# Kernel optimization log

Hardware: AMD Instinct MI355X
Metric: run time of the kernel (lower is better)

## Reference

```python
import jax, jax.numpy as jnp
import numpy as np

N_NODES = 100000
N_EDGES = 1600000
F_IN, F_HID, F_OUT = 128, 128, 16


def _add_self_loops(edge_index, n):
    loop = jnp.arange(n, dtype=edge_index.dtype)
    src = jnp.concatenate([edge_index[0], loop])
    dst = jnp.concatenate([edge_index[1], loop])
    return src, dst


def _gcn_conv(x, W, b, src, dst, n):
    # linear transform first (PyG/jraphx GCNConv order)
    h = x @ W  # [N, out]
    # symmetric normalization with unit edge weights, degrees on dst (incl. self loops)
    ones = jnp.ones(src.shape[0], dtype=h.dtype)
    deg = jax.ops.segment_sum(ones, dst, num_segments=n)
    dinv = jnp.where(deg > 0, jax.lax.rsqrt(deg), jnp.zeros((), h.dtype))
    norm = dinv[src] * dinv[dst]  # [E']
    msg = h[src] * norm[:, None]  # gather + scale: [E', out]
    out = jax.ops.segment_sum(msg, dst, num_segments=n)  # scatter-add
    return out + b


def setup_inputs() -> dict:
    key = jax.random.key(0)
    k1, k2, k3, k4, k5, k6 = jax.random.split(key, 6)
    x = jax.random.normal(k1, (N_NODES, F_IN), dtype=jnp.float32)
    edge_index = jax.random.randint(k2, (2, N_EDGES), 0, N_NODES, dtype=jnp.int32)
    W1 = jax.random.normal(k3, (F_IN, F_HID), dtype=jnp.float32) * (1.0 / np.sqrt(F_IN))
    b1 = jnp.zeros((F_HID,), dtype=jnp.float32)
    W2 = jax.random.normal(k4, (F_HID, F_OUT), dtype=jnp.float32) * (1.0 / np.sqrt(F_HID))
    b2 = jnp.zeros((F_OUT,), dtype=jnp.float32)
    return {"x": x, "edge_index": edge_index, "W1": W1, "b1": b1, "W2": W2, "b2": b2}


def reference(x, edge_index, W1, b1, W2, b2):
    n = x.shape[0]
    src, dst = _add_self_loops(edge_index, n)
    h = _gcn_conv(x, W1, b1, src, dst, n)
    h = jax.nn.relu(h)
    # dropout is identity in eval mode
    return _gcn_conv(h, W2, b2, src, dst, n)
```

## Files before the change

kernel.cpp:

```cpp
#include <hip/hip_runtime.h>
#include <hip/hip_fp16.h>

#define NN 100000
#define NE 1600000
#define ETOT (NE + NN)
#define FIN 128
#define FHID 128
#define FOUT 16

#define NB1 196
#define PBLK 256
#define PCH (NE / PBLK)
#define P2_CAP 10240

typedef _Float16 f16x8 __attribute__((ext_vector_type(8)));
typedef float f32x4 __attribute__((ext_vector_type(4)));


__global__ __launch_bounds__(256) void k_cnt(const int* __restrict__ ei,
                                             const float* __restrict__ W1,
                                             int* __restrict__ cnt,
                                             _Float16* __restrict__ WT) {
    int tid = threadIdx.x, blk = blockIdx.x;
    if (blk < PBLK) {
        __shared__ int h[NB1];
        for (int i = tid; i < NB1; i += 256) h[i] = 0;
        __syncthreads();
        const int* dst = ei + NE;
        int e0 = blk * PCH;
        for (int e = e0 + tid; e < e0 + PCH; e += 256)
            atomicAdd(&h[dst[e] >> 9], 1);
        __syncthreads();
        for (int i = tid; i < NB1; i += 256) cnt[blk * NB1 + i] = h[i];
    } else {
        __shared__ _Float16 tl[16][136];
        int b = blk - PBLK;
        #pragma unroll
        for (int i = 0; i < 8; ++i) {
            int idx = tid + i * 256;
            int k = idx >> 7, n = idx & 127;
            tl[k][n] = (_Float16)W1[(b * 16 + k) * FHID + n];
        }
        __syncthreads();
        #pragma unroll
        for (int i = 0; i < 8; ++i) {
            int idx = tid + i * 256;
            int n = idx >> 4, k = idx & 15;
            WT[n * FIN + b * 16 + k] = tl[k][n];
        }
    }
}

__global__ __launch_bounds__(256) void k_offs(const int* __restrict__ cnt,
                                              int* __restrict__ woffp,
                                              int* __restrict__ bintot,
                                              int* __restrict__ rowptr) {
    __shared__ int s[256];
    int b = blockIdx.x;
    int t = threadIdx.x;
    int v = cnt[t * NB1 + b];
    s[t] = v;
    __syncthreads();
    for (int off = 1; off < 256; off <<= 1) {
        int xv = (t >= off) ? s[t - off] : 0;
        __syncthreads();
        s[t] += xv;
        __syncthreads();
    }
    woffp[t * NB1 + b] = s[t] - v;
    if (t == 255) bintot[b] = s[255];
    if (b == 0 && t == 0) rowptr[NN] = ETOT;
}

__global__ __launch_bounds__(256) void k_scat(const int* __restrict__ ei,
                                              const int* __restrict__ woffp,
                                              const int* __restrict__ bintot,
                                              unsigned* __restrict__ binned) {
    __shared__ int sc[256];
    __shared__ int cur[NB1];
    int tid = threadIdx.x;
    int k = blockIdx.x;
    int v = (tid < NB1) ? bintot[tid] : 0;
    sc[tid] = v;
    __syncthreads();
    for (int off = 1; off < 256; off <<= 1) {
        int xv = (tid >= off) ? sc[tid - off] : 0;
        __syncthreads();
        sc[tid] += xv;
        __syncthreads();
    }
    if (tid < NB1) cur[tid] = (sc[tid] - v) + woffp[k * NB1 + tid];
    __syncthreads();
    int e0 = k * PCH;
    for (int e = e0 + tid; e < e0 + PCH; e += 256) {
        int s = ei[e], d = ei[NE + e];
        int b = d >> 9;
        int pos = atomicAdd(&cur[b], 1);
        binned[pos] = (unsigned)s | ((unsigned)(d & 511) << 17);
    }
}

__global__ __launch_bounds__(256) void k_build(const unsigned* __restrict__ binned,
                                               const int* __restrict__ bintot,
                                               int* __restrict__ rowptr,
                                               float* __restrict__ dinv,
                                               int* __restrict__ col) {
    __shared__ int dcnt[512];
    __shared__ int pref[512];
    __shared__ int sc[256];
    __shared__ int ord[P2_CAP];
    int blk = blockIdx.x;
    int tid = threadIdx.x;
    int bv = (tid < NB1) ? bintot[tid] : 0;
    sc[tid] = bv;
    __syncthreads();
    for (int off = 1; off < 256; off <<= 1) {
        int xv = (tid >= off) ? sc[tid - off] : 0;
        __syncthreads();
        sc[tid] += xv;
        __syncthreads();
    }
    int ecnt = bintot[blk];
    int eb = sc[blk] - ecnt;
    __syncthreads();
    int n0 = blk * 512;
    int nn = min(512, NN - n0);
    int colbase = eb + n0;
    dcnt[tid] = 0; dcnt[tid + 256] = 0;
    __syncthreads();
    for (int e = tid; e < ecnt; e += 256)
        atomicAdd(&dcnt[binned[eb + e] >> 17], 1);
    __syncthreads();
    int d0 = (2 * tid < nn)     ? dcnt[2 * tid] + 1     : 0;
    int d1 = (2 * tid + 1 < nn) ? dcnt[2 * tid + 1] + 1 : 0;
    sc[tid] = d0 + d1;
    __syncthreads();
    for (int off = 1; off < 256; off <<= 1) {
        int xv = (tid >= off) ? sc[tid - off] : 0;
        __syncthreads();
        sc[tid] += xv;
        __syncthreads();
    }
    int base = sc[tid] - d0 - d1;
    pref[2 * tid] = base;
    pref[2 * tid + 1] = base + d0;
    __syncthreads();
    for (int i = tid; i < nn; i += 256) {
        int p = pref[i];
        rowptr[n0 + i] = colbase + p;
        dinv[n0 + i] = rsqrtf((float)(dcnt[i] + 1));
        ord[p] = n0 + i;
    }
    __syncthreads();
    for (int i = tid; i < nn; i += 256) dcnt[i] = pref[i] + 1;
    __syncthreads();
    for (int e = tid; e < ecnt; e += 256) {
        unsigned p = binned[eb + e];
        int pos = atomicAdd(&dcnt[p >> 17], 1);
        int sv = (int)(p & 0x1FFFFu);
        if (pos < P2_CAP) ord[pos] = sv; else col[colbase + pos] = sv;
    }
    __syncthreads();
    int tot = ecnt + nn;
    int lim = min(tot, P2_CAP);
    for (int i = tid; i < lim; i += 256) col[colbase + i] = ord[i];
}


__global__ __launch_bounds__(256) void k_gemm1(const float* __restrict__ x,
                                               const _Float16* __restrict__ WT,
                                               const float* __restrict__ dinv,
                                               _Float16* __restrict__ h) {
    __shared__ _Float16 xs[64 * 128];
    __shared__ _Float16 ws[128 * 128];
    int tid = threadIdx.x;
    int m0 = blockIdx.x * 64;
    #pragma unroll
    for (int i = 0; i < 4; ++i) {
        int u = tid + i * 256;
        int r = u >> 4;
        int k0 = (u & 15) * 8;
        int row = m0 + r;
        f16x8 v = {};
        if (row < NN) {
            float4 a = *(const float4*)&x[(size_t)row * FIN + k0];
            float4 b = *(const float4*)&x[(size_t)row * FIN + k0 + 4];
            v[0] = (_Float16)a.x; v[1] = (_Float16)a.y;
            v[2] = (_Float16)a.z; v[3] = (_Float16)a.w;
            v[4] = (_Float16)b.x; v[5] = (_Float16)b.y;
            v[6] = (_Float16)b.z; v[7] = (_Float16)b.w;
        }
        *(f16x8*)&xs[r * 128 + (k0 ^ ((r & 7) * 8))] = v;
    }
    #pragma unroll
    for (int i = 0; i < 8; ++i) {
        int u = tid + i * 256;
        int n = u >> 4;
        int k0 = (u & 15) * 8;
        f16x8 v = *(const f16x8*)&WT[n * FIN + k0];
        *(f16x8*)&ws[n * 128 + (k0 ^ ((n & 7) * 8))] = v;
    }
    __syncthreads();
    int wave = tid >> 6, lane = tid & 63;
    int lm = lane & 15, lg = lane >> 4;
    f32x4 acc[8];
    #pragma unroll
    for (int t = 0; t < 8; ++t) acc[t] = (f32x4){0.f, 0.f, 0.f, 0.f};
    int am = wave * 16 + lm;
    #pragma unroll
    for (int s = 0; s < 4; ++s) {
        int ka = s * 32 + lg * 8;
        f16x8 af = *(const f16x8*)&xs[am * 128 + (ka ^ ((am & 7) * 8))];
        #pragma unroll
        for (int t = 0; t < 8; ++t) {
            int bn = t * 16 + lm;
            f16x8 bf = *(const f16x8*)&ws[bn * 128 + (ka ^ ((bn & 7) * 8))];
            acc[t] = __builtin_amdgcn_mfma_f32_16x16x32_f16(af, bf, acc[t], 0, 0, 0);
        }
    }
    float dsc[4];
    #pragma unroll
    for (int r = 0; r < 4; ++r) {
        int grow = m0 + wave * 16 + lg * 4 + r;
        dsc[r] = (grow < NN) ? dinv[grow] : 0.f;
    }
    #pragma unroll
    for (int t = 0; t < 8; ++t) {
        int coln = t * 16 + lm;
        #pragma unroll
        for (int r = 0; r < 4; ++r) {
            int grow = m0 + wave * 16 + lg * 4 + r;
            if (grow < NN)
                h[(size_t)grow * FHID + coln] = (_Float16)(acc[t][r] * dsc[r]);
        }
    }
}


__device__ __forceinline__ void add_row8(float* acc, int4 raw) {
    const __half2* p = reinterpret_cast<const __half2*>(&raw);
    #pragma unroll
    for (int j = 0; j < 4; ++j) {
        float2 f = __half22float2(p[j]);
        acc[2 * j]     += f.x;
        acc[2 * j + 1] += f.y;
    }
}


__global__ __launch_bounds__(256) void k_agg1(const __half2* __restrict__ hf,
                                              const int* __restrict__ rowptr,
                                              const int* __restrict__ col,
                                              const float* __restrict__ dinv,
                                              const float* __restrict__ b1,
                                              __half2* __restrict__ out1) {
    int tid = threadIdx.x;
    int node = blockIdx.x * 16 + (tid >> 4);
    int lane = tid & 15;
    int beg = rowptr[node];
    int end = rowptr[node + 1];
    float acc[8] = {};
    int e = beg;
    for (; e + 4 <= end; e += 4) {
        int s0 = col[e], s1 = col[e + 1], s2 = col[e + 2], s3 = col[e + 3];
        int4 r0 = *reinterpret_cast<const int4*>(hf + (size_t)s0 * 64 + lane * 4);
        int4 r1 = *reinterpret_cast<const int4*>(hf + (size_t)s1 * 64 + lane * 4);
        int4 r2 = *reinterpret_cast<const int4*>(hf + (size_t)s2 * 64 + lane * 4);
        int4 r3 = *reinterpret_cast<const int4*>(hf + (size_t)s3 * 64 + lane * 4);
        add_row8(acc, r0);
        add_row8(acc, r1);
        add_row8(acc, r2);
        add_row8(acc, r3);
    }
    for (; e < end; ++e) {
        int s = col[e];
        int4 r = *reinterpret_cast<const int4*>(hf + (size_t)s * 64 + lane * 4);
        add_row8(acc, r);
    }
    float di = dinv[node];
    float4 bA = *(const float4*)&b1[lane * 8];
    float4 bB = *(const float4*)&b1[lane * 8 + 4];
    float o[8];
    o[0] = fmaxf(acc[0] * di + bA.x, 0.f);
    o[1] = fmaxf(acc[1] * di + bA.y, 0.f);
    o[2] = fmaxf(acc[2] * di + bA.z, 0.f);
    o[3] = fmaxf(acc[3] * di + bA.w, 0.f);
    o[4] = fmaxf(acc[4] * di + bB.x, 0.f);
    o[5] = fmaxf(acc[5] * di + bB.y, 0.f);
    o[6] = fmaxf(acc[6] * di + bB.z, 0.f);
    o[7] = fmaxf(acc[7] * di + bB.w, 0.f);
    __half2 ph[4];
    #pragma unroll
    for (int j = 0; j < 4; ++j) ph[j] = __floats2half2_rn(o[2 * j], o[2 * j + 1]);
    *reinterpret_cast<int4*>(out1 + (size_t)node * 64 + lane * 4) =
        *reinterpret_cast<int4*>(ph);
}


__global__ __launch_bounds__(256) void k_gemm2(const _Float16* __restrict__ a,
                                               const float* __restrict__ W,
                                               const float* __restrict__ dinv,
                                               _Float16* __restrict__ h2) {
    __shared__ _Float16 w2t[16][136];
    int tid = threadIdx.x;
    #pragma unroll
    for (int i = 0; i < 8; ++i) {
        int idx = tid + i * 256;
        w2t[idx & 15][idx >> 4] = (_Float16)W[idx];
    }
    __syncthreads();
    int wave = tid >> 6, lane = tid & 63;
    int lm = lane & 15, lg = lane >> 4;
    f16x8 bf[4];
    #pragma unroll
    for (int s = 0; s < 4; ++s)
        bf[s] = *(const f16x8*)&w2t[lm][s * 32 + lg * 8];
    int row0 = blockIdx.x * 256 + wave * 64;
    #pragma unroll
    for (int rt = 0; rt < 4; ++rt) {
        int rbase = row0 + rt * 16;
        f32x4 acc = {0.f, 0.f, 0.f, 0.f};
        #pragma unroll
        for (int s = 0; s < 4; ++s) {
            int arow = rbase + lm;
            f16x8 af = {};
            if (arow < NN)
                af = *(const f16x8*)&a[(size_t)arow * FHID + s * 32 + lg * 8];
            acc = __builtin_amdgcn_mfma_f32_16x16x32_f16(af, bf[s], acc, 0, 0, 0);
        }
        #pragma unroll
        for (int r = 0; r < 4; ++r) {
            int row = rbase + lg * 4 + r;
            if (row < NN)
                h2[(size_t)row * FOUT + lm] = (_Float16)(acc[r] * dinv[row]);
        }
    }
}


__global__ __launch_bounds__(256) void k_agg2(const __half2* __restrict__ h2,
                                              const int* __restrict__ rowptr,
                                              const int* __restrict__ col,
                                              const float* __restrict__ dinv,
                                              const float* __restrict__ b2,
                                              float* __restrict__ out) {
    int tid = threadIdx.x;
    int node = blockIdx.x * 128 + (tid >> 1);
    if (node >= NN) return;
    int l = tid & 1;
    int beg = rowptr[node];
    int end = rowptr[node + 1];
    float acc[8] = {};
    int e = beg;
    for (; e + 4 <= end; e += 4) {
        int s0 = col[e], s1 = col[e + 1], s2 = col[e + 2], s3 = col[e + 3];
        int4 r0 = *reinterpret_cast<const int4*>(h2 + (size_t)s0 * 8 + l * 4);
        int4 r1 = *reinterpret_cast<const int4*>(h2 + (size_t)s1 * 8 + l * 4);
        int4 r2 = *reinterpret_cast<const int4*>(h2 + (size_t)s2 * 8 + l * 4);
        int4 r3 = *reinterpret_cast<const int4*>(h2 + (size_t)s3 * 8 + l * 4);
        add_row8(acc, r0);
        add_row8(acc, r1);
        add_row8(acc, r2);
        add_row8(acc, r3);
    }
    for (; e < end; ++e) {
        int s = col[e];
        int4 r = *reinterpret_cast<const int4*>(h2 + (size_t)s * 8 + l * 4);
        add_row8(acc, r);
    }
    float di = dinv[node];
    float4 bA = *(const float4*)&b2[l * 8];
    float4 bB = *(const float4*)&b2[l * 8 + 4];
    float4 oA, oB;
    oA.x = acc[0] * di + bA.x;  oA.y = acc[1] * di + bA.y;
    oA.z = acc[2] * di + bA.z;  oA.w = acc[3] * di + bA.w;
    oB.x = acc[4] * di + bB.x;  oB.y = acc[5] * di + bB.y;
    oB.z = acc[6] * di + bB.z;  oB.w = acc[7] * di + bB.w;
    *(float4*)&out[(size_t)node * 16 + l * 8] = oA;
    *(float4*)&out[(size_t)node * 16 + l * 8 + 4] = oB;
}


extern "C" void kernel_launch(void* const* d_in, const int* in_sizes, int n_in,
                              void* d_out, int out_size, void* d_ws, size_t ws_size,
                              hipStream_t stream) {
    const float* x  = (const float*)d_in[0];
    const int*   ei = (const int*)d_in[1];
    const float* W1 = (const float*)d_in[2];
    const float* b1 = (const float*)d_in[3];
    const float* W2 = (const float*)d_in[4];
    const float* b2 = (const float*)d_in[5];
    float* out = (float*)d_out;

    char* ws = (char*)d_ws;
    size_t off = 0;
    #define WS_ALLOC(ptr_t, name, bytes) \
        ptr_t name = (ptr_t)(ws + off); off = (off + (size_t)(bytes) + 511) & ~(size_t)511;
    WS_ALLOC(int*,       rowptr,   ((size_t)NN + 1) * 4)
    WS_ALLOC(int*,       cnt,      (size_t)PBLK * NB1 * 4)
    WS_ALLOC(int*,       woffp,    (size_t)PBLK * NB1 * 4)
    WS_ALLOC(int*,       bintot,   (size_t)NB1 * 4)
    WS_ALLOC(int*,       colv,     (size_t)ETOT * 4)
    WS_ALLOC(float*,     dinv,     (size_t)NN * 4)
    WS_ALLOC(_Float16*,  w1t,      (size_t)FIN * FHID * 2)
    WS_ALLOC(_Float16*,  hf,       (size_t)NN * FHID * 2)
    WS_ALLOC(__half2*,   out1f,    (size_t)NN * FHID * 2)
    WS_ALLOC(_Float16*,  h2f,      (size_t)NN * FOUT * 2)
    #undef WS_ALLOC
    (void)ws_size; (void)in_sizes; (void)n_in; (void)out_size;

    unsigned* binned = (unsigned*)hf;

    k_cnt<<<PBLK + 8, 256, 0, stream>>>(ei, W1, cnt, w1t);
    k_offs<<<NB1, 256, 0, stream>>>(cnt, woffp, bintot, rowptr);
    k_scat<<<PBLK, 256, 0, stream>>>(ei, woffp, bintot, binned);
    k_build<<<NB1, 256, 0, stream>>>(binned, bintot, rowptr, dinv, colv);

    k_gemm1<<<(NN + 63) / 64, 256, 0, stream>>>(x, w1t, dinv, hf);
    k_agg1<<<NN / 16, 256, 0, stream>>>((const __half2*)hf, rowptr, colv, dinv, b1, out1f);

    k_gemm2<<<(NN + 255) / 256, 256, 0, stream>>>((const _Float16*)out1f, W2, dinv, h2f);
    k_agg2<<<(NN + 127) / 128, 256, 0, stream>>>((const __half2*)h2f, rowptr, colv, dinv, b2, out);
}
```

Before: 167.6 us.

## Fuse second-layer linear transform into first aggregation epilogue

The layer-1 aggregation kernel now multiplies its ReLU output by W2, staged in shared memory, and reduces across 16 lanes with shuffles. It writes the 16-wide pre-scaled h2 directly. This removes the separate GEMM kernel and the full 128-wide intermediate write and reread. In exchange it adds per-node scalar FMAs, shuffle reductions and a shared-memory weight load per block to the gather kernel.

```diff
diff --git a/kernel.cpp b/kernel.cpp
--- a/kernel.cpp
+++ b/kernel.cpp
@@ -253,8 +253,16 @@
                                               const int* __restrict__ col,
                                               const float* __restrict__ dinv,
                                               const float* __restrict__ b1,
-                                              __half2* __restrict__ out1) {
+                                              const float* __restrict__ W2,
+                                              _Float16* __restrict__ h2) {
+    __shared__ _Float16 w2s[128][17];
     int tid = threadIdx.x;
+    #pragma unroll
+    for (int i = 0; i < 8; ++i) {
+        int idx = tid + i * 256;
+        w2s[idx >> 4][idx & 15] = (_Float16)W2[idx];
+    }
+    __syncthreads();
     int node = blockIdx.x * 16 + (tid >> 4);
     int lane = tid & 15;
     int beg = rowptr[node];
@@ -289,52 +297,24 @@
     o[5] = fmaxf(acc[5] * di + bB.y, 0.f);
     o[6] = fmaxf(acc[6] * di + bB.z, 0.f);
     o[7] = fmaxf(acc[7] * di + bB.w, 0.f);
-    __half2 ph[4];
-    #pragma unroll
-    for (int j = 0; j < 4; ++j) ph[j] = __floats2half2_rn(o[2 * j], o[2 * j + 1]);
-    *reinterpret_cast<int4*>(out1 + (size_t)node * 64 + lane * 4) =
-        *reinterpret_cast<int4*>(ph);
-}
-
-
-__global__ __launch_bounds__(256) void k_gemm2(const _Float16* __restrict__ a,
-                                               const float* __restrict__ W,
-                                               const float* __restrict__ dinv,
-                                               _Float16* __restrict__ h2) {
-    __shared__ _Float16 w2t[16][136];
-    int tid = threadIdx.x;
-    #pragma unroll
-    for (int i = 0; i < 8; ++i) {
-        int idx = tid + i * 256;
-        w2t[idx & 15][idx >> 4] = (_Float16)W[idx];
-    }
-    __syncthreads();
-    int wave = tid >> 6, lane = tid & 63;
-    int lm = lane & 15, lg = lane >> 4;
-    f16x8 bf[4];
-    #pragma unroll
-    for (int s = 0; s < 4; ++s)
-        bf[s] = *(const f16x8*)&w2t[lm][s * 32 + lg * 8];
-    int row0 = blockIdx.x * 256 + wave * 64;
-    #pragma unroll
-    for (int rt = 0; rt < 4; ++rt) {
-        int rbase = row0 + rt * 16;
-        f32x4 acc = {0.f, 0.f, 0.f, 0.f};
-        #pragma unroll
-        for (int s = 0; s < 4; ++s) {
-            int arow = rbase + lm;
-            f16x8 af = {};
-            if (arow < NN)
-                af = *(const f16x8*)&a[(size_t)arow * FHID + s * 32 + lg * 8];
-            acc = __builtin_amdgcn_mfma_f32_16x16x32_f16(af, bf[s], acc, 0, 0, 0);
-        }
-        #pragma unroll
-        for (int r = 0; r < 4; ++r) {
-            int row = rbase + lg * 4 + r;
-            if (row < NN)
-                h2[(size_t)row * FOUT + lm] = (_Float16)(acc[r] * dinv[row]);
-        }
-    }
+    float v[16];
+    #pragma unroll
+    for (int c = 0; c < 16; ++c) {
+        float s = 0.f;
+        #pragma unroll
+        for (int j = 0; j < 8; ++j)
+            s += o[j] * (float)w2s[lane * 8 + j][c];
+        v[c] = s;
+    }
+    #pragma unroll
+    for (int m = 8; m >= 1; m >>= 1)
+        #pragma unroll
+        for (int c = 0; c < 16; ++c)
+            v[c] += __shfl_xor(v[c], m, 16);
+    float r = v[0];
+    #pragma unroll
+    for (int c = 1; c < 16; ++c) r = (lane == c) ? v[c] : r;
+    h2[(size_t)node * FOUT + lane] = (_Float16)(r * di);
 }
 
 
@@ -404,7 +384,6 @@
     WS_ALLOC(float*,     dinv,     (size_t)NN * 4)
     WS_ALLOC(_Float16*,  w1t,      (size_t)FIN * FHID * 2)
     WS_ALLOC(_Float16*,  hf,       (size_t)NN * FHID * 2)
-    WS_ALLOC(__half2*,   out1f,    (size_t)NN * FHID * 2)
     WS_ALLOC(_Float16*,  h2f,      (size_t)NN * FOUT * 2)
     #undef WS_ALLOC
     (void)ws_size; (void)in_sizes; (void)n_in; (void)out_size;
@@ -417,8 +396,9 @@
     k_build<<<NB1, 256, 0, stream>>>(binned, bintot, rowptr, dinv, colv);
 
     k_gemm1<<<(NN + 63) / 64, 256, 0, stream>>>(x, w1t, dinv, hf);
-    k_agg1<<<NN / 16, 256, 0, stream>>>((const __half2*)hf, rowptr, colv, dinv, b1, out1f);
-
-    k_gemm2<<<(NN + 255) / 256, 256, 0, stream>>>((const _Float16*)out1f, W2, dinv, h2f);
-    k_agg2<<<(NN + 127) / 128, 256, 0, stream>>>((const __half2*)h2f, rowptr, colv, dinv, b2, out);
-}
+    k_agg1<<<NN / 16, 256, 0, stream>>>((const __half2*)hf, rowptr, colv, dinv,
+                                        b1, W2, h2f);
+
+    k_agg2<<<(NN + 127) / 128, 256, 0, stream>>>((const __half2*)h2f, rowptr,
+                                                 colv, dinv, b2, out);
+}
```

Measured after the change: 187.3 us. +11.8%, slower.
